# Kernel optimization log

Hardware: AMD Instinct MI355X
Metric: run time of the kernel (lower is better)

## Reference

```python
import jax, jax.numpy as jnp
import numpy as np

N_LAYERS = 101  # 1 initial conv+relu + 100 appended conv+relu pairs

def setup_inputs() -> dict:
    key = jax.random.key(0)
    kx, kw, kb = jax.random.split(key, 3)
    x = jax.random.normal(kx, (32, 1, 1024, 1024), dtype=jnp.float32)
    # Each Conv2d(1,1,1) has a scalar weight and scalar bias. Keep weights
    # near 1 and biases small so the 101-deep chain stays numerically sane.
    w = 1.0 + 0.02 * jax.random.normal(kw, (N_LAYERS,), dtype=jnp.float32)
    b = 0.01 * jax.random.normal(kb, (N_LAYERS,), dtype=jnp.float32)
    return {"x": x, "w": w, "b": b}

def reference(x, w, b):
    def step(h, wb):
        wi, bi = wb
        return jax.nn.relu(h * wi + bi), None
    out, _ = jax.lax.scan(step, x, (w, b))
    return out
```

## Files before the change

### kernel.cpp

```cpp
#include <hip/hip_runtime.h>
#include <math.h>

#define N_LAYERS 101

__global__ __launch_bounds__(256) void fused_chain(
    const float4* __restrict__ x4,
    const float* __restrict__ x,
    const float* __restrict__ w,
    const float* __restrict__ b,
    float4* __restrict__ o4,
    float* __restrict__ o,
    int n4, int n) {
    __shared__ float ws[N_LAYERS];
    __shared__ float bs[N_LAYERS];
    for (int i = threadIdx.x; i < N_LAYERS; i += blockDim.x) {
        ws[i] = w[i];
        bs[i] = b[i];
    }
    __syncthreads();

    float A = ws[0], B = bs[0], C = 0.0f;
    bool ok = true;
    for (int i = 1; i < N_LAYERS; ++i) {
        const float wi = ws[i], bi = bs[i];
        ok = ok && (wi >= 0.0f);
        A = wi * A;
        B = fmaf(wi, B, bi);
        C = fmaxf(fmaf(wi, C, bi), 0.0f);
    }

    const int tid = blockIdx.x * blockDim.x + threadIdx.x;
    const int stride = gridDim.x * blockDim.x;

    if (ok) {
        for (int i = tid; i < n4; i += stride) {
            float4 v = x4[i];
            v.x = fmaxf(fmaf(A, v.x, B), C);
            v.y = fmaxf(fmaf(A, v.y, B), C);
            v.z = fmaxf(fmaf(A, v.z, B), C);
            v.w = fmaxf(fmaf(A, v.w, B), C);
            o4[i] = v;
        }
        for (int i = n4 * 4 + tid; i < n; i += stride) {
            o[i] = fmaxf(fmaf(A, x[i], B), C);
        }
    } else {
        #pragma unroll 1
        for (int i = tid; i < n4; i += stride) {
            float4 v = x4[i];
            #pragma unroll 1
            for (int l = 0; l < N_LAYERS; ++l) {
                const float wl = ws[l], bl = bs[l];
                v.x = fmaxf(fmaf(wl, v.x, bl), 0.0f);
                v.y = fmaxf(fmaf(wl, v.y, bl), 0.0f);
                v.z = fmaxf(fmaf(wl, v.z, bl), 0.0f);
                v.w = fmaxf(fmaf(wl, v.w, bl), 0.0f);
            }
            o4[i] = v;
        }
        #pragma unroll 1
        for (int i = n4 * 4 + tid; i < n; i += stride) {
            float v = x[i];
            #pragma unroll 1
            for (int l = 0; l < N_LAYERS; ++l) {
                v = fmaxf(fmaf(ws[l], v, bs[l]), 0.0f);
            }
            o[i] = v;
        }
    }
}

extern "C" void kernel_launch(void* const* d_in, const int* in_sizes, int n_in,
                              void* d_out, int out_size, void* d_ws, size_t ws_size,
                              hipStream_t stream) {
    const float* x = (const float*)d_in[0];
    const float* w = (const float*)d_in[1];
    const float* b = (const float*)d_in[2];
    float* out = (float*)d_out;

    const int n  = in_sizes[0];
    const int n4 = n / 4;

    int blocks = (n4 + 255) / 256;
    if (blocks > 2048) blocks = 2048;
    fused_chain<<<blocks, 256, 0, stream>>>(
        (const float4*)x, x, w, b, (float4*)out, out, n4, n);
}
```

Before: 237.7 us.

## Precompute collapsed affine in a tiny kernel; one-shot grid with nontemporal stores

Moves the 101-layer collapse into a separate single-block kernel that writes A, B, C and a fast-path flag to workspace, so the main kernel no longer repeats the serial chain in every block. The main kernel drops the grid-stride loop and launches one block per 1024 float4s, with each thread issuing four independent loads up front and writing results with nontemporal stores. This adds a second kernel launch and a dependent global read of the coefficients, and it launches many more blocks than the previous 2048 cap.

```diff
diff --git a/kernel.cpp b/kernel.cpp
--- a/kernel.cpp
+++ b/kernel.cpp
@@ -3,51 +3,79 @@
 
 #define N_LAYERS 101
 
-__global__ __launch_bounds__(256) void fused_chain(
-    const float4* __restrict__ x4,
+typedef float f32x4 __attribute__((ext_vector_type(4)));
+
+__global__ void collapse_abc(const float* __restrict__ w,
+                             const float* __restrict__ b,
+                             float* __restrict__ abc) {
+    __shared__ float ws[N_LAYERS];
+    __shared__ float bs[N_LAYERS];
+    const int t = threadIdx.x;
+    if (t < N_LAYERS) { ws[t] = w[t]; bs[t] = b[t]; }
+    __syncthreads();
+    if (t == 0) {
+        float A = ws[0], B = bs[0], C = 0.0f, ok = 1.0f;
+        for (int i = 1; i < N_LAYERS; ++i) {
+            const float wi = ws[i], bi = bs[i];
+            if (wi < 0.0f) ok = 0.0f;
+            A = wi * A;
+            B = fmaf(wi, B, bi);
+            C = fmaxf(fmaf(wi, C, bi), 0.0f);
+        }
+        abc[0] = A; abc[1] = B; abc[2] = C; abc[3] = ok;
+    }
+    if (t < N_LAYERS) {
+        abc[8 + t] = w[t];
+        abc[8 + N_LAYERS + t] = b[t];
+    }
+}
+
+__global__ __launch_bounds__(256) void apply_affine(
+    const f32x4* __restrict__ x4,
     const float* __restrict__ x,
-    const float* __restrict__ w,
-    const float* __restrict__ b,
-    float4* __restrict__ o4,
+    const float* __restrict__ abc,
+    f32x4* __restrict__ o4,
     float* __restrict__ o,
     int n4, int n) {
     __shared__ float ws[N_LAYERS];
     __shared__ float bs[N_LAYERS];
-    for (int i = threadIdx.x; i < N_LAYERS; i += blockDim.x) {
-        ws[i] = w[i];
-        bs[i] = b[i];
-    }
-    __syncthreads();
 
-    float A = ws[0], B = bs[0], C = 0.0f;
-    bool ok = true;
-    for (int i = 1; i < N_LAYERS; ++i) {
-        const float wi = ws[i], bi = bs[i];
-        ok = ok && (wi >= 0.0f);
-        A = wi * A;
-        B = fmaf(wi, B, bi);
-        C = fmaxf(fmaf(wi, C, bi), 0.0f);
-    }
+    const float A = abc[0], B = abc[1], C = abc[2];
+    const bool fast = (abc[3] != 0.0f);
 
-    const int tid = blockIdx.x * blockDim.x + threadIdx.x;
-    const int stride = gridDim.x * blockDim.x;
+    const int gtid = blockIdx.x * blockDim.x + threadIdx.x;
+    const int gsz  = gridDim.x * blockDim.x;
 
-    if (ok) {
-        for (int i = tid; i < n4; i += stride) {
-            float4 v = x4[i];
-            v.x = fmaxf(fmaf(A, v.x, B), C);
-            v.y = fmaxf(fmaf(A, v.y, B), C);
-            v.z = fmaxf(fmaf(A, v.z, B), C);
+    if (fast) {
+        const int i0 = blockIdx.x * 1024 + threadIdx.x;
+        const int i1 = i0 + 256, i2 = i0 + 512, i3 = i0 + 768;
+        f32x4 v0, v1, v2, v3;
+        if (i0 < n4) v0 = x4[i0];
+        if (i1 < n4) v1 = x4[i1];
+        if (i2 < n4) v2 = x4[i2];
+        if (i3 < n4) v3 = x4[i3];
+        #define APPLY(v) \
+            v.x = fmaxf(fmaf(A, v.x, B), C); \
+            v.y = fmaxf(fmaf(A, v.y, B), C); \
+            v.z = fmaxf(fmaf(A, v.z, B), C); \
             v.w = fmaxf(fmaf(A, v.w, B), C);
-            o4[i] = v;
-        }
-        for (int i = n4 * 4 + tid; i < n; i += stride) {
+        if (i0 < n4) { APPLY(v0); __builtin_nontemporal_store(v0, &o4[i0]); }
+        if (i1 < n4) { APPLY(v1); __builtin_nontemporal_store(v1, &o4[i1]); }
+        if (i2 < n4) { APPLY(v2); __builtin_nontemporal_store(v2, &o4[i2]); }
+        if (i3 < n4) { APPLY(v3); __builtin_nontemporal_store(v3, &o4[i3]); }
+        #undef APPLY
+        for (int i = n4 * 4 + gtid; i < n; i += gsz) {
             o[i] = fmaxf(fmaf(A, x[i], B), C);
         }
     } else {
+        for (int i = threadIdx.x; i < N_LAYERS; i += blockDim.x) {
+            ws[i] = abc[8 + i];
+            bs[i] = abc[8 + N_LAYERS + i];
+        }
+        __syncthreads();
         #pragma unroll 1
-        for (int i = tid; i < n4; i += stride) {
-            float4 v = x4[i];
+        for (int i = gtid; i < n4; i += gsz) {
+            f32x4 v = x4[i];
             #pragma unroll 1
             for (int l = 0; l < N_LAYERS; ++l) {
                 const float wl = ws[l], bl = bs[l];
@@ -59,7 +87,7 @@
             o4[i] = v;
         }
         #pragma unroll 1
-        for (int i = n4 * 4 + tid; i < n; i += stride) {
+        for (int i = n4 * 4 + gtid; i < n; i += gsz) {
             float v = x[i];
             #pragma unroll 1
             for (int l = 0; l < N_LAYERS; ++l) {
@@ -77,12 +105,14 @@
     const float* w = (const float*)d_in[1];
     const float* b = (const float*)d_in[2];
     float* out = (float*)d_out;
+    float* abc = (float*)d_ws;
 
     const int n  = in_sizes[0];
     const int n4 = n / 4;
 
-    int blocks = (n4 + 255) / 256;
-    if (blocks > 2048) blocks = 2048;
-    fused_chain<<<blocks, 256, 0, stream>>>(
-        (const float4*)x, x, w, b, (float4*)out, out, n4, n);
+    collapse_abc<<<1, 128, 0, stream>>>(w, b, abc);
+
+    const int blocks = (n4 + 1023) / 1024;
+    apply_affine<<<blocks, 256, 0, stream>>>(
+        (const f32x4*)x, x, abc, (f32x4*)out, out, n4, n);
 }
```

Measured after the change: 237.7 us. About the same (+0.0%).

## Prefetch sixteen vectors per thread with nontemporal access before coefficient folding

Applied to the files above, without the earlier changes.

Each block now owns a fixed contiguous span, and each thread issues sixteen nontemporal vector loads up front, before folding the 101 scalar coefficients into one affine-plus-clamp. This overlaps the serial coefficient computation with memory latency and keeps many loads in flight per thread. It also drops the shared-memory staging and barrier on the fast path by reading the coefficients straight from global memory. Nontemporal stores avoid polluting caches. The trade-off is higher register pressure, and a partial last block falls back to a guarded loop.

```diff
diff --git a/kernel.cpp b/kernel.cpp
--- a/kernel.cpp
+++ b/kernel.cpp
@@ -3,51 +3,104 @@
 
 #define N_LAYERS 101
 
-__global__ __launch_bounds__(256) void fused_chain(
-    const float4* __restrict__ x4,
+typedef float f32x4 __attribute__((ext_vector_type(4)));
+
+#define PER_THREAD 16
+#define BLOCK_SPAN (256 * PER_THREAD)
+
+__global__ __launch_bounds__(256) void apply_affine(
+    const f32x4* __restrict__ x4,
     const float* __restrict__ x,
     const float* __restrict__ w,
     const float* __restrict__ b,
-    float4* __restrict__ o4,
+    f32x4* __restrict__ o4,
     float* __restrict__ o,
     int n4, int n) {
-    __shared__ float ws[N_LAYERS];
-    __shared__ float bs[N_LAYERS];
-    for (int i = threadIdx.x; i < N_LAYERS; i += blockDim.x) {
-        ws[i] = w[i];
-        bs[i] = b[i];
+    const int t    = threadIdx.x;
+    const int base = blockIdx.x * BLOCK_SPAN + t;
+    const bool full = (int)((blockIdx.x + 1) * BLOCK_SPAN) <= n4;
+
+    f32x4 v0, v1, v2, v3, v4, v5, v6, v7, v8, v9, v10, v11, v12, v13, v14, v15;
+    if (full) {
+        v0  = __builtin_nontemporal_load(x4 + base + 0  * 256);
+        v1  = __builtin_nontemporal_load(x4 + base + 1  * 256);
+        v2  = __builtin_nontemporal_load(x4 + base + 2  * 256);
+        v3  = __builtin_nontemporal_load(x4 + base + 3  * 256);
+        v4  = __builtin_nontemporal_load(x4 + base + 4  * 256);
+        v5  = __builtin_nontemporal_load(x4 + base + 5  * 256);
+        v6  = __builtin_nontemporal_load(x4 + base + 6  * 256);
+        v7  = __builtin_nontemporal_load(x4 + base + 7  * 256);
+        v8  = __builtin_nontemporal_load(x4 + base + 8  * 256);
+        v9  = __builtin_nontemporal_load(x4 + base + 9  * 256);
+        v10 = __builtin_nontemporal_load(x4 + base + 10 * 256);
+        v11 = __builtin_nontemporal_load(x4 + base + 11 * 256);
+        v12 = __builtin_nontemporal_load(x4 + base + 12 * 256);
+        v13 = __builtin_nontemporal_load(x4 + base + 13 * 256);
+        v14 = __builtin_nontemporal_load(x4 + base + 14 * 256);
+        v15 = __builtin_nontemporal_load(x4 + base + 15 * 256);
     }
-    __syncthreads();
 
-    float A = ws[0], B = bs[0], C = 0.0f;
+    float A = w[0], B = b[0], C = 0.0f;
     bool ok = true;
     for (int i = 1; i < N_LAYERS; ++i) {
-        const float wi = ws[i], bi = bs[i];
+        const float wi = w[i], bi = b[i];
         ok = ok && (wi >= 0.0f);
         A = wi * A;
         B = fmaf(wi, B, bi);
         C = fmaxf(fmaf(wi, C, bi), 0.0f);
     }
 
-    const int tid = blockIdx.x * blockDim.x + threadIdx.x;
-    const int stride = gridDim.x * blockDim.x;
-
     if (ok) {
-        for (int i = tid; i < n4; i += stride) {
-            float4 v = x4[i];
-            v.x = fmaxf(fmaf(A, v.x, B), C);
-            v.y = fmaxf(fmaf(A, v.y, B), C);
-            v.z = fmaxf(fmaf(A, v.z, B), C);
+        #define APPLY(v) \
+            v.x = fmaxf(fmaf(A, v.x, B), C); \
+            v.y = fmaxf(fmaf(A, v.y, B), C); \
+            v.z = fmaxf(fmaf(A, v.z, B), C); \
             v.w = fmaxf(fmaf(A, v.w, B), C);
-            o4[i] = v;
+        if (full) {
+            APPLY(v0);  __builtin_nontemporal_store(v0,  o4 + base + 0  * 256);
+            APPLY(v1);  __builtin_nontemporal_store(v1,  o4 + base + 1  * 256);
+            APPLY(v2);  __builtin_nontemporal_store(v2,  o4 + base + 2  * 256);
+            APPLY(v3);  __builtin_nontemporal_store(v3,  o4 + base + 3  * 256);
+            APPLY(v4);  __builtin_nontemporal_store(v4,  o4 + base + 4  * 256);
+            APPLY(v5);  __builtin_nontemporal_store(v5,  o4 + base + 5  * 256);
+            APPLY(v6);  __builtin_nontemporal_store(v6,  o4 + base + 6  * 256);
+            APPLY(v7);  __builtin_nontemporal_store(v7,  o4 + base + 7  * 256);
+            APPLY(v8);  __builtin_nontemporal_store(v8,  o4 + base + 8  * 256);
+            APPLY(v9);  __builtin_nontemporal_store(v9,  o4 + base + 9  * 256);
+            APPLY(v10); __builtin_nontemporal_store(v10, o4 + base + 10 * 256);
+            APPLY(v11); __builtin_nontemporal_store(v11, o4 + base + 11 * 256);
+            APPLY(v12); __builtin_nontemporal_store(v12, o4 + base + 12 * 256);
+            APPLY(v13); __builtin_nontemporal_store(v13, o4 + base + 13 * 256);
+            APPLY(v14); __builtin_nontemporal_store(v14, o4 + base + 14 * 256);
+            APPLY(v15); __builtin_nontemporal_store(v15, o4 + base + 15 * 256);
+        } else {
+            #pragma unroll 1
+            for (int k = 0; k < PER_THREAD; ++k) {
+                const int i = base + k * 256;
+                if (i < n4) {
+                    f32x4 v = __builtin_nontemporal_load(x4 + i);
+                    APPLY(v);
+                    __builtin_nontemporal_store(v, o4 + i);
+                }
+            }
+            for (int i = n4 * 4 + t; i < n; i += 256) {
+                o[i] = fmaxf(fmaf(A, x[i], B), C);
+            }
         }
-        for (int i = n4 * 4 + tid; i < n; i += stride) {
-            o[i] = fmaxf(fmaf(A, x[i], B), C);
+        #undef APPLY
+    } else {
+        __shared__ float ws[N_LAYERS];
+        __shared__ float bs[N_LAYERS];
+        for (int i = t; i < N_LAYERS; i += blockDim.x) {
+            ws[i] = w[i];
+            bs[i] = b[i];
         }
-    } else {
+        __syncthreads();
+        const int gtid = blockIdx.x * blockDim.x + t;
+        const int gsz  = gridDim.x * blockDim.x;
         #pragma unroll 1
-        for (int i = tid; i < n4; i += stride) {
-            float4 v = x4[i];
+        for (int i = gtid; i < n4; i += gsz) {
+            f32x4 v = x4[i];
             #pragma unroll 1
             for (int l = 0; l < N_LAYERS; ++l) {
                 const float wl = ws[l], bl = bs[l];
@@ -59,7 +112,7 @@
             o4[i] = v;
         }
         #pragma unroll 1
-        for (int i = n4 * 4 + tid; i < n; i += stride) {
+        for (int i = n4 * 4 + gtid; i < n; i += gsz) {
             float v = x[i];
             #pragma unroll 1
             for (int l = 0; l < N_LAYERS; ++l) {
@@ -81,8 +134,8 @@
     const int n  = in_sizes[0];
     const int n4 = n / 4;
 
-    int blocks = (n4 + 255) / 256;
-    if (blocks > 2048) blocks = 2048;
-    fused_chain<<<blocks, 256, 0, stream>>>(
-        (const float4*)x, x, w, b, (float4*)out, out, n4, n);
+    int blocks = (n4 + BLOCK_SPAN - 1) / BLOCK_SPAN;
+    if (blocks < 1) blocks = 1;
+    apply_affine<<<blocks, 256, 0, stream>>>(
+        (const f32x4*)x, x, w, b, (f32x4*)out, out, n4, n);
 }
```

After: 223.3 us. -6.1%, faster.
